# Performance work log

Hardware: AMD Instinct MI355X
Metric: run time of the kernel (lower is better)

## Reference

```python
import jax, jax.numpy as jnp
import numpy as np

INPUT_DIM = 1024
HIDDEN_DIM = 2048
NUM_BLOCKS = 8
BLOCK_SIZE = HIDDEN_DIM // NUM_BLOCKS
BATCH = 2048


def setup_inputs() -> dict:
    key = jax.random.key(0)
    ks = jax.random.split(key, 6)
    # PyTorch GRUCell init: uniform(-1/sqrt(hidden_size), 1/sqrt(hidden_size))
    bound = 1.0 / np.sqrt(BLOCK_SIZE)
    u = lambda k, shape: jax.random.uniform(k, shape, jnp.float32, -bound, bound)
    return {
        "input": jax.random.normal(ks[0], (BATCH, INPUT_DIM), jnp.float32),
        "hidden": jax.random.normal(ks[1], (BATCH, HIDDEN_DIM), jnp.float32),
        # stacked per-block GRUCell params (block-diagonal structure)
        "W_ih": u(ks[2], (NUM_BLOCKS, 3 * BLOCK_SIZE, INPUT_DIM)),
        "W_hh": u(ks[3], (NUM_BLOCKS, 3 * BLOCK_SIZE, BLOCK_SIZE)),
        "b_ih": u(ks[4], (NUM_BLOCKS, 3 * BLOCK_SIZE)),
        "b_hh": u(ks[5], (NUM_BLOCKS, 3 * BLOCK_SIZE)),
    }


def reference(input, hidden, W_ih, W_hh, b_ih, b_hh):
    B = input.shape[0]
    nb, g3, bs = W_hh.shape  # [num_blocks, 3*block_size, block_size]
    hb = hidden.reshape(B, nb, bs)                      # [B, nb, bs]
    # input-to-gate and hidden-to-gate projections, batched over blocks
    gi = jnp.einsum("bi,ngi->bng", input, W_ih) + b_ih  # [B, nb, 3*bs]
    gh = jnp.einsum("bns,ngs->bng", hb, W_hh) + b_hh    # [B, nb, 3*bs]
    i_r, i_z, i_n = jnp.split(gi, 3, axis=-1)
    h_r, h_z, h_n = jnp.split(gh, 3, axis=-1)
    r = jax.nn.sigmoid(i_r + h_r)
    z = jax.nn.sigmoid(i_z + h_z)
    n = jnp.tanh(i_n + r * h_n)
    new_h = (1.0 - z) * n + z * hb                      # [B, nb, bs]
    return new_h.reshape(B, nb * bs)
```

## Files before the change

### kernel.cpp

```cpp
#include <hip/hip_runtime.h>
#include <hip/hip_bf16.h>
#include <type_traits>

#define AS1 __attribute__((address_space(1)))
#define AS3 __attribute__((address_space(3)))

typedef __attribute__((ext_vector_type(4))) float f32x4;
typedef __attribute__((ext_vector_type(8))) short bf16x8;

template <int V> using ic = std::integral_constant<int, V>;

static constexpr int B_   = 2048;
static constexpr int IN_  = 1024;
static constexpr int HID_ = 2048;
static constexpr int NB_  = 8;
static constexpr int BS_  = 256;
static constexpr int G3_  = 768;

__device__ __forceinline__ unsigned cvtpk(float lo, float hi) {
  unsigned r;
  asm("v_cvt_pk_bf16_f32 %0, %1, %2" : "=v"(r) : "v"(lo), "v"(hi));
  return r;
}

__device__ __forceinline__ unsigned short f2bf(float f) {
  unsigned u = __builtin_bit_cast(unsigned, f);
  u = (u + 0x7FFFu + ((u >> 16) & 1u)) >> 16;
  return (unsigned short)u;
}

__global__ void cvt_w(const float* __restrict__ Wih, const float* __restrict__ Whh,
                      unsigned short* __restrict__ dst) {
  constexpr int c0 = (NB_ * G3_ * IN_) / 4;
  constexpr int n4 = c0 + (NB_ * G3_ * BS_) / 4;
  int i = blockIdx.x * blockDim.x + threadIdx.x;
  int stride = gridDim.x * blockDim.x;
  for (; i < n4; i += stride) {
    float4 v = (i < c0) ? reinterpret_cast<const float4*>(Wih)[i]
                        : reinterpret_cast<const float4*>(Whh)[i - c0];
    ushort4 o;
    o.x = f2bf(v.x); o.y = f2bf(v.y); o.z = f2bf(v.z); o.w = f2bf(v.w);
    reinterpret_cast<ushort4*>(dst)[i] = o;
  }
}

__global__ __launch_bounds__(256, 2) void gru_mfma(
    const float* __restrict__ xf,
    const float* __restrict__ hf,
    const unsigned short* __restrict__ wihb,
    const unsigned short* __restrict__ whhb,
    const float* __restrict__ b_ih,
    const float* __restrict__ b_hh,
    float* __restrict__ out)
{
  __shared__ __align__(16) char lds[2][40960];

  const int t    = threadIdx.x;
  const int lane = t & 63;
  const int wid  = t >> 6;
  const int wm   = wid >> 1;
  const int wn   = wid & 1;

  const int bid = blockIdx.x;
  const int swz = (bid & 7) * 64 + (bid >> 3);
  const int mrow0 = (swz & 15) * 128;
  const int ct    = swz >> 4;
  const int n     = ct >> 2;
  const int s0    = (ct & 3) * 64;

  int arow[4], acolE[4];
#pragma unroll
  for (int p = 0; p < 4; ++p) {
    int op = p * 4096 + t * 16;
    int ol = op ^ (((op >> 7) & 7) << 4);
    arow[p]  = ol >> 7;
    acolE[p] = (ol & 127) >> 1;
  }
  int wgrow[6], wcb[6];
#pragma unroll
  for (int q = 0; q < 6; ++q) {
    int op = q * 4096 + t * 16;
    int ol = op ^ (((op >> 7) & 7) << 4);
    int wr = ol >> 7;
    wgrow[q] = n * G3_ + (wr >> 6) * BS_ + s0 + (wr & 63);
    wcb[q]   = ol & 127;
  }

  f32x4 acc[4][4][2] = {};
  float4 sa[4][2];

  auto issueA = [&](int t2) {
#pragma unroll
    for (int p = 0; p < 4; ++p) {
      const float* src = (t2 < 16)
        ? xf + (size_t)(mrow0 + arow[p]) * IN_  + t2 * 64 + acolE[p]
        : hf + (size_t)(mrow0 + arow[p]) * HID_ + n * BS_ + (t2 - 16) * 64 + acolE[p];
      sa[p][0] = *reinterpret_cast<const float4*>(src);
      sa[p][1] = *reinterpret_cast<const float4*>(src + 4);
    }
  };
  auto stageW = [&](int buf, int t2) {
    const bool ph1 = t2 < 16;
    const int ks = ph1 ? t2 : (t2 - 16);
    char* base = (char*)lds[buf] + 16384;
#pragma unroll
    for (int q = 0; q < 6; ++q) {
      const char* src = ph1
        ? (const char*)wihb + ((size_t)wgrow[q] * IN_ + ks * 64) * 2 + wcb[q]
        : (const char*)whhb + ((size_t)wgrow[q] * BS_ + ks * 64) * 2 + wcb[q];
      __builtin_amdgcn_global_load_lds((const AS1 void*)src,
                                       (AS3 void*)(base + q * 4096 + wid * 1024), 16, 0, 0);
    }
  };
  auto pack8 = [&](const float4& a, const float4& b) {
    union { unsigned u[4]; bf16x8 v; } r;
    r.u[0] = cvtpk(a.x, a.y); r.u[1] = cvtpk(a.z, a.w);
    r.u[2] = cvtpk(b.x, b.y); r.u[3] = cvtpk(b.z, b.w);
    return r.v;
  };
  auto writeA = [&](int buf) {
    char* base = (char*)lds[buf];
#pragma unroll
    for (int p = 0; p < 4; ++p)
      *reinterpret_cast<bf16x8*>(base + p * 4096 + t * 16) = pack8(sa[p][0], sa[p][1]);
  };

  auto loadA = [&](const char* buf, bf16x8 (&af)[2][4]) {
#pragma unroll
    for (int ksub = 0; ksub < 2; ++ksub)
#pragma unroll
      for (int mi = 0; mi < 4; ++mi) {
        int ar  = wm * 64 + mi * 16 + (lane & 15);
        int off = ar * 128 + ksub * 64 + ((lane >> 4) * 16);
        off ^= (ar & 7) << 4;
        af[ksub][mi] = *reinterpret_cast<const bf16x8*>(buf + off);
      }
  };
  auto loadW = [&](const char* buf, int g, bf16x8 (&wf)[2][2]) {
#pragma unroll
    for (int ksub = 0; ksub < 2; ++ksub)
#pragma unroll
      for (int ni = 0; ni < 2; ++ni) {
        int wr  = g * 64 + wn * 32 + ni * 16 + (lane & 15);
        int off = wr * 128 + ksub * 64 + ((lane >> 4) * 16);
        off ^= (wr & 7) << 4;
        wf[ksub][ni] = *reinterpret_cast<const bf16x8*>(buf + 16384 + off);
      }
  };
  auto mfmaSet = [&](auto setc, bf16x8 (&af)[2][4], bf16x8 (&wf)[2][2]) {
    constexpr int set = decltype(setc)::value;
    __builtin_amdgcn_s_setprio(1);
#pragma unroll
    for (int ksub = 0; ksub < 2; ++ksub)
#pragma unroll
      for (int mi = 0; mi < 4; ++mi)
#pragma unroll
        for (int ni = 0; ni < 2; ++ni)
          acc[set][mi][ni] = __builtin_amdgcn_mfma_f32_16x16x32_bf16(
              af[ksub][mi], wf[ksub][ni], acc[set][mi][ni], 0, 0, 0);
    __builtin_amdgcn_s_setprio(0);
  };

  issueA(0);
  stageW(0, 0);
  writeA(0);
  __syncthreads();

#pragma unroll
  for (int tt = 0; tt < 20; ++tt) {
    const char* cur = (const char*)lds[tt & 1];
    const int oth = (tt & 1) ^ 1;
    bf16x8 af[2][4], wf[2][2];

    if (tt < 19) { issueA(tt + 1); stageW(oth, tt + 1); }
    __builtin_amdgcn_sched_barrier(0);

    loadA(cur, af);
    loadW(cur, 0, wf); mfmaSet(ic<0>{}, af, wf);
    loadW(cur, 1, wf); mfmaSet(ic<1>{}, af, wf);
    loadW(cur, 2, wf);
    if (tt < 16) mfmaSet(ic<2>{}, af, wf);
    else         mfmaSet(ic<3>{}, af, wf);

    __builtin_amdgcn_sched_barrier(0);
    if (tt < 19) writeA(oth);
    __syncthreads();
  }

#pragma unroll
  for (int ni = 0; ni < 2; ++ni) {
    int scol = s0 + wn * 32 + ni * 16 + (lane & 15);
    float br_i = b_ih[n * G3_ + 0 * BS_ + scol];
    float bz_i = b_ih[n * G3_ + 1 * BS_ + scol];
    float bn_i = b_ih[n * G3_ + 2 * BS_ + scol];
    float br_h = b_hh[n * G3_ + 0 * BS_ + scol];
    float bz_h = b_hh[n * G3_ + 1 * BS_ + scol];
    float bn_h = b_hh[n * G3_ + 2 * BS_ + scol];
    int gcol = n * BS_ + scol;
#pragma unroll
    for (int mi = 0; mi < 4; ++mi) {
#pragma unroll
      for (int i = 0; i < 4; ++i) {
        int row = mrow0 + wm * 64 + mi * 16 + (lane >> 4) * 4 + i;
        float hprev = hf[(size_t)row * HID_ + gcol];
        float rr = acc[0][mi][ni][i] + br_i + br_h;
        float zz = acc[1][mi][ni][i] + bz_i + bz_h;
        float r  = 1.f / (1.f + __expf(-rr));
        float z  = 1.f / (1.f + __expf(-zz));
        float ng = tanhf(acc[2][mi][ni][i] + bn_i + r * (acc[3][mi][ni][i] + bn_h));
        out[(size_t)row * HID_ + gcol] = (1.f - z) * ng + z * hprev;
      }
    }
  }
}

__global__ void gru_naive(const float* __restrict__ x, const float* __restrict__ h,
                          const float* __restrict__ Wih, const float* __restrict__ Whh,
                          const float* __restrict__ bih, const float* __restrict__ bhh,
                          float* __restrict__ out) {
  int b = blockIdx.x;
  int n = blockIdx.y;
  int s = threadIdx.x;
  __shared__ float xs[1024];
  __shared__ float hs[256];
  for (int i = threadIdx.x; i < 1024; i += 256) xs[i] = x[(size_t)b * IN_ + i];
  if (threadIdx.x < 256) hs[threadIdx.x] = h[(size_t)b * HID_ + n * BS_ + threadIdx.x];
  __syncthreads();
  float gi[3], gh[3];
  for (int g = 0; g < 3; ++g) {
    const float* w = Wih + ((size_t)(n * G3_ + g * BS_ + s)) * IN_;
    float a = 0.f;
    for (int k = 0; k < IN_; ++k) a += xs[k] * w[k];
    gi[g] = a + bih[n * G3_ + g * BS_ + s];
    const float* w2 = Whh + ((size_t)(n * G3_ + g * BS_ + s)) * BS_;
    float a2 = 0.f;
    for (int k = 0; k < BS_; ++k) a2 += hs[k] * w2[k];
    gh[g] = a2 + bhh[n * G3_ + g * BS_ + s];
  }
  float r = 1.f / (1.f + expf(-(gi[0] + gh[0])));
  float z = 1.f / (1.f + expf(-(gi[1] + gh[1])));
  float ng = tanhf(gi[2] + r * gh[2]);
  out[(size_t)b * HID_ + n * BS_ + s] = (1.f - z) * ng + z * hs[s];
}

extern "C" void kernel_launch(void* const* d_in, const int* in_sizes, int n_in,
                              void* d_out, int out_size, void* d_ws, size_t ws_size,
                              hipStream_t stream) {
  const float* x   = (const float*)d_in[0];
  const float* h   = (const float*)d_in[1];
  const float* Wih = (const float*)d_in[2];
  const float* Whh = (const float*)d_in[3];
  const float* bih = (const float*)d_in[4];
  const float* bhh = (const float*)d_in[5];
  float* out = (float*)d_out;

  const size_t szwih = (size_t)NB_ * G3_ * IN_;
  const size_t szwhh = (size_t)NB_ * G3_ * BS_;
  const size_t need  = (szwih + szwhh) * 2;

  if (ws_size >= need) {
    unsigned short* wihb = (unsigned short*)d_ws;
    unsigned short* whhb = wihb + szwih;
    cvt_w<<<1024, 256, 0, stream>>>(Wih, Whh, wihb);
    gru_mfma<<<512, 256, 0, stream>>>(x, h, wihb, whhb, bih, bhh, out);
  } else {
    dim3 grid(B_, NB_);
    gru_naive<<<grid, 256, 0, stream>>>(x, h, Wih, Whh, bih, bhh, out);
  }
}
```

Measured before the change: 56.06 us.

## Deepen global-to-LDS prefetch to two tiles ahead with explicit waitcnt barriers

```diff
diff --git a/kernel.cpp b/kernel.cpp
--- a/kernel.cpp
+++ b/kernel.cpp
@@ -163,16 +163,24 @@
 
   issueA(0);
   stageW(0, 0);
+  asm volatile("s_waitcnt vmcnt(6)");
+  __builtin_amdgcn_sched_barrier(0);
   writeA(0);
-  __syncthreads();
+  issueA(1);
+  stageW(1, 1);
+  asm volatile("s_waitcnt vmcnt(6)");
+  __builtin_amdgcn_sched_barrier(0);
+  writeA(1);
+  asm volatile("s_waitcnt lgkmcnt(0)");
+  __builtin_amdgcn_sched_barrier(0);
+  __builtin_amdgcn_s_barrier();
 
 #pragma unroll
   for (int tt = 0; tt < 20; ++tt) {
     const char* cur = (const char*)lds[tt & 1];
-    const int oth = (tt & 1) ^ 1;
     bf16x8 af[2][4], wf[2][2];
 
-    if (tt < 19) { issueA(tt + 1); stageW(oth, tt + 1); }
+    if (tt + 2 < 20) issueA(tt + 2);
     __builtin_amdgcn_sched_barrier(0);
 
     loadA(cur, af);
@@ -182,9 +190,24 @@
     if (tt < 16) mfmaSet(ic<2>{}, af, wf);
     else         mfmaSet(ic<3>{}, af, wf);
 
+    asm volatile("s_waitcnt lgkmcnt(0)");
     __builtin_amdgcn_sched_barrier(0);
-    if (tt < 19) writeA(oth);
-    __syncthreads();
+    __builtin_amdgcn_s_barrier();
+
+    if (tt + 2 < 20) {
+      asm volatile("s_waitcnt vmcnt(0)");
+      __builtin_amdgcn_sched_barrier(0);
+      writeA(tt & 1);
+      stageW(tt & 1, tt + 2);
+      asm volatile("s_waitcnt lgkmcnt(0)");
+      __builtin_amdgcn_sched_barrier(0);
+    }
+    if (tt < 19) {
+      if (tt + 2 < 20) asm volatile("s_waitcnt vmcnt(6)");
+      else             asm volatile("s_waitcnt vmcnt(0)");
+      __builtin_amdgcn_sched_barrier(0);
+      __builtin_amdgcn_s_barrier();
+    }
   }
 
 #pragma unroll
```

Result: no change. 55.63 us (-0.8%).
